# Optimization experiments

Measured on AMD Instinct MI355X. Metric: run time of the kernel, lower is better.

## Reference

```python
import jax, jax.numpy as jnp
import numpy as np

# graph / model dims
N0, N1, N2 = 200000, 50000, 10000   # nodes per sampled layer (src of hop0, src of hop1, targets)
L = 10                               # tokens per node for embedding sum
E0, E1 = 800000, 160000              # edges per hop
V, IN, H, U, LP = 100000, 128, 256, 32, 128  # vocab, in_channels, hidden, unsup_channels, predictor hidden


def _ln(x, g, b, eps=1e-5):
    m = jnp.mean(x, axis=-1, keepdims=True)
    v = jnp.var(x, axis=-1, keepdims=True)
    return (x - m) * jax.lax.rsqrt(v + eps) * g + b


def _lp_edge(e_i, e_j, w1, b1, g, b, w2, b2):
    # LabelPredictor.edge_forward (eval mode: no dropout)
    h = jnp.concatenate([jnp.abs(e_i - e_j), e_i + e_j, e_i * e_j], axis=-1)  # [E, 3U]
    h = jax.nn.relu(_ln(h @ w1.T + b1, g, b))                                  # [E, LP]
    return jax.nn.sigmoid(h @ w2.T + b2)                                       # [E, 1]


def _conv(x_src, x_tgt, src, dst, n_dst, in_c, ll_w, ll_b, lr_w, lp):
    # LAConv.propagate + message, aggr='add', bipartite (x_src, x_tgt)
    xj = x_src[src]                    # gather [E, in_c+U]
    feat_j = xj[:, :in_c]
    un_j = xj[:, in_c:]
    un_i = x_tgt[dst, in_c:]
    A = jax.lax.stop_gradient(_lp_edge(un_i, un_j, *lp))       # [E, 1], frozen predictor
    A_sum = jax.ops.segment_sum(A, dst, num_segments=n_dst)    # softmax-like normalizer
    A = A / A_sum[dst]
    msg = jnp.concatenate([A * feat_j, un_j], axis=-1)         # [E, in_c+U]
    out = jax.ops.segment_sum(msg, dst, num_segments=n_dst)    # scatter-add aggregate
    out_feat = out[:, :in_c] @ ll_w.T + ll_b + x_tgt[:, :in_c] @ lr_w.T
    return jnp.concatenate([out_feat, out[:, in_c:]], axis=-1)


def setup_inputs() -> dict:
    key = jax.random.key(0)
    ks = jax.random.split(key, 24)
    f = lambda k, shape, s=0.02: (jax.random.normal(k, shape, dtype=jnp.float32) * s)
    inp = {
        'x': jax.random.randint(ks[0], (N0, L), 0, V),
        'x_unsup': jax.random.normal(ks[1], (N0, U), dtype=jnp.float32),
        'src0': jax.random.randint(ks[2], (E0,), 0, N0),
        'dst0': jax.random.randint(ks[3], (E0,), 0, N1),
        'src1': jax.random.randint(ks[4], (E1,), 0, N1),
        'dst1': jax.random.randint(ks[5], (E1,), 0, N2),
        'emb_table': f(ks[6], (V, IN), 1.0),
        'ln_g': jnp.ones((IN,), jnp.float32),
        'ln_b': jnp.zeros((IN,), jnp.float32),
        'lp_w1': f(ks[7], (LP, 3 * U), 0.05),
        'lp_b1': jnp.zeros((LP,), jnp.float32),
        'lp_g': jnp.ones((LP,), jnp.float32),
        'lp_bn': jnp.zeros((LP,), jnp.float32),
        'lp_w2': f(ks[8], (1, LP), 0.05),
        'lp_b2': jnp.zeros((1,), jnp.float32),
        'll_w0': f(ks[9], (H, IN)),
        'll_b0': jnp.zeros((H,), jnp.float32),
        'lr_w0': f(ks[10], (H, IN)),
        'll_w1': f(ks[11], (H, H)),
        'll_b1': jnp.zeros((H,), jnp.float32),
        'lr_w1': f(ks[12], (H, H)),
        'out_w': f(ks[13], (1, H)),
        'out_b': jnp.zeros((1,), jnp.float32),
    }
    return inp


def reference(x, x_unsup, src0, dst0, src1, dst1, emb_table, ln_g, ln_b,
              lp_w1, lp_b1, lp_g, lp_bn, lp_w2, lp_b2,
              ll_w0, ll_b0, lr_w0, ll_w1, ll_b1, lr_w1, out_w, out_b):
    lp = (lp_w1, lp_b1, lp_g, lp_bn, lp_w2, lp_b2)
    # embedding with padding_idx=0 (row 0 contributes zero)
    mask = jnp.concatenate([jnp.zeros((1, 1), jnp.float32), jnp.ones((V - 1, 1), jnp.float32)], axis=0)
    table = emb_table * mask
    e = jnp.sum(table[x], axis=1)                 # [N0, IN]
    e = jax.nn.relu(_ln(e, ln_g, ln_b))
    h = jnp.concatenate([e, x_unsup], axis=-1)    # [N0, IN+U]

    # layer 0 (IN -> H)
    h = _conv(h, h[:N1], src0, dst0, N1, IN, ll_w0, ll_b0, lr_w0, lp)
    feat, un = h[:, :H], h[:, H:]
    h = jnp.concatenate([jax.nn.relu(feat), un], axis=-1)  # eval: no dropout

    # layer 1 (H -> H), last layer: no relu
    h = _conv(h, h[:N2], src1, dst1, N2, H, ll_w1, ll_b1, lr_w1, lp)

    return h[:, :H] @ out_w.T + out_b             # [N2, 1]
```

## Files before the change

kernel.cpp:

```cpp
#include <hip/hip_runtime.h>
#include <hip/hip_bf16.h>
#include <math.h>

#define cN0 200000
#define cN1 50000
#define cN2 10000
#define cL  10
#define cE0 800000
#define cE1 160000
#define cV  100000
#define cIN 128
#define cH  256
#define cU  32
#define cLP 128

typedef __attribute__((ext_vector_type(8))) short short8;
typedef __attribute__((ext_vector_type(4))) float floatx4;

__device__ __forceinline__ float wave_sum(float v) {
#pragma unroll
    for (int m = 1; m < 64; m <<= 1) v += __shfl_xor(v, m);
    return v;
}

__device__ __forceinline__ float red16(float v) {
    v += __shfl_xor(v, 1); v += __shfl_xor(v, 2);
    v += __shfl_xor(v, 4); v += __shfl_xor(v, 8);
    return v;
}

__device__ __forceinline__ unsigned short bf16_rne(float f) {
    union { float f; unsigned u; } c; c.f = f;
    unsigned r = (c.u + 0x7FFFu + ((c.u >> 16) & 1u)) >> 16;
    return (unsigned short)r;
}

__device__ __forceinline__ float b2f(unsigned short u) {
    union { unsigned u; float f; } c; c.u = ((unsigned)u) << 16;
    return c.f;
}

__device__ __forceinline__ unsigned pkbf16(float a, float b) {
    union { __hip_bfloat162 h; unsigned u; } c;
    c.h = __float22bfloat162_rn(make_float2(a, b));
    return c.u;
}

__device__ __forceinline__ float2 unpk(unsigned p) {
    union { unsigned u; float f; } lo, hi;
    lo.u = p << 16; hi.u = p & 0xFFFF0000u;
    return make_float2(lo.f, hi.f);
}

__global__ __launch_bounds__(256) void cvt4_kernel(const float* __restrict__ src,
                                                   ushort* __restrict__ dstp)
{
    size_t i = ((size_t)blockIdx.x * 256 + threadIdx.x) * 4;
    float4 v = *(const float4*)&src[i];
    unsigned o0 = pkbf16(v.x, v.y), o1 = pkbf16(v.z, v.w);
    *(uint2*)&dstp[i] = make_uint2(o0, o1);
}

__global__ __launch_bounds__(256) void cvt_w0_kernel(const float* __restrict__ llw0,
                                                     const float* __restrict__ lrw0,
                                                     ushort* __restrict__ Wb)
{
    int idx = blockIdx.x * 256 + threadIdx.x;
    int i = idx * 2;
    int o = i >> 8, k = i & 255;
    float2 v = (k < 128) ? *(const float2*)&llw0[o * 128 + k]
                         : *(const float2*)&lrw0[o * 128 + (k - 128)];
    *(unsigned*)&Wb[i] = pkbf16(v.x, v.y);
}

__global__ __launch_bounds__(256) void embed_kernel(
    const int* __restrict__ x, const ushort* __restrict__ embB,
    const float* __restrict__ g, const float* __restrict__ b,
    ushort* __restrict__ e0)
{
    int wave = threadIdx.x >> 6, lane = threadIdx.x & 63;
    int n = blockIdx.x * 4 + wave;
    const int* xr = x + (size_t)n * cL;
    int toks[cL];
#pragma unroll
    for (int t = 0; t < cL; ++t) toks[t] = xr[t];
    unsigned packed[cL];
#pragma unroll
    for (int t = 0; t < cL; ++t)
        packed[t] = *(const unsigned*)&embB[(size_t)toks[t] * cIN + 2 * lane];
    float ax = 0.f, ay = 0.f;
#pragma unroll
    for (int t = 0; t < cL; ++t) {
        unsigned p = (toks[t] != 0) ? packed[t] : 0u;
        float2 uv = unpk(p);
        ax += uv.x; ay += uv.y;
    }
    float s1 = wave_sum(ax + ay);
    float s2 = wave_sum(ax * ax + ay * ay);
    float mean = s1 * (1.f / cIN);
    float var = s2 * (1.f / cIN) - mean * mean;
    float rstd = rsqrtf(var + 1e-5f);
    float2 gv = *(const float2*)&g[2 * lane];
    float2 bv = *(const float2*)&b[2 * lane];
    float ox = fmaxf((ax - mean) * rstd * gv.x + bv.x, 0.f);
    float oy = fmaxf((ay - mean) * rstd * gv.y + bv.y, 0.f);
    *(unsigned*)&e0[(size_t)n * cIN + 2 * lane] = pkbf16(ox, oy);
}

__global__ void count_kernel(const int* __restrict__ dst, int E, int* __restrict__ cnt)
{
    int e = blockIdx.x * 256 + threadIdx.x;
    if (e < E) atomicAdd(&cnt[dst[e]], 1);
}

__global__ __launch_bounds__(1024) void scan_kernel(const int* __restrict__ cnt,
                                                    int* __restrict__ off, int n)
{
    __shared__ int ps[1024];
    int t = threadIdx.x;
    int chunk = (n + 1023) / 1024;
    int lo = t * chunk;
    int hi = min(lo + chunk, n);
    int s = 0;
    for (int i = lo; i < hi; ++i) s += cnt[i];
    ps[t] = s;
    __syncthreads();
    for (int d = 1; d < 1024; d <<= 1) {
        int v = (t >= d) ? ps[t - d] : 0;
        __syncthreads();
        ps[t] += v;
        __syncthreads();
    }
    int run = ps[t] - s;
    for (int i = lo; i < hi; ++i) { off[i] = run; run += cnt[i]; }
    if (hi == n) off[n] = run;
}

__global__ void scatter_kernel(const int* __restrict__ dst, int E,
                               const int* __restrict__ off, int* __restrict__ pos,
                               int* __restrict__ eid)
{
    int e = blockIdx.x * 256 + threadIdx.x;
    if (e < E) {
        int d = dst[e];
        int p = atomicAdd(&pos[d], 1);
        eid[off[d] + p] = e;
    }
}

__global__ __launch_bounds__(256) void edge_mlp_mfma_kernel(
    const ushort* __restrict__ uni, int stride_i,
    const ushort* __restrict__ unj, int stride_j,
    const int* __restrict__ src, const int* __restrict__ dst, int E,
    const float* __restrict__ w1, const float* __restrict__ b1v,
    const float* __restrict__ gv, const float* __restrict__ bnv,
    const float* __restrict__ w2, const float* __restrict__ b2,
    float* __restrict__ A)
{
    __shared__ float par[cLP * 4];
    int tid = threadIdx.x;
    if (tid < cLP) {
        par[tid * 4 + 0] = b1v[tid];
        par[tid * 4 + 1] = gv[tid];
        par[tid * 4 + 2] = bnv[tid];
        par[tid * 4 + 3] = w2[tid];
    }
    int lane = tid & 63;
    int n = lane & 15, q = lane >> 4;

    union { short8 s; unsigned u[4]; } Bf[8][3];
#pragma unroll
    for (int nt = 0; nt < 8; ++nt) {
#pragma unroll
        for (int c = 0; c < 3; ++c) {
            const float* p = &w1[(size_t)(16 * nt + n) * 96 + 32 * c + 8 * q];
            float4 v0 = *(const float4*)p;
            float4 v1 = *(const float4*)(p + 4);
            Bf[nt][c].u[0] = pkbf16(v0.x, v0.y);
            Bf[nt][c].u[1] = pkbf16(v0.z, v0.w);
            Bf[nt][c].u[2] = pkbf16(v1.x, v1.y);
            Bf[nt][c].u[3] = pkbf16(v1.z, v1.w);
        }
    }
    __syncthreads();
    float b2s = b2[0];

    int wid = blockIdx.x * 4 + (tid >> 6);
    int nw = gridDim.x * 4;
    int ngroups = E >> 4;

    int g = wid;
    int di = 0, si = 0;
    if (g < ngroups) {
        int e = (g << 4) + n;
        di = dst[e]; si = src[e];
    }
    while (g < ngroups) {
        uint4 ivu = *(const uint4*)&uni[(size_t)di * stride_i + 8 * q];
        uint4 jvu = *(const uint4*)&unj[(size_t)si * stride_j + 8 * q];
        int gn = g + nw;
        if (gn < ngroups) {
            int e2 = (gn << 4) + n;
            di = dst[e2]; si = src[e2];
        }
        union { short8 s; unsigned u[4]; } a0, a1, a2;
        {
            unsigned iw[4] = {ivu.x, ivu.y, ivu.z, ivu.w};
            unsigned jw[4] = {jvu.x, jvu.y, jvu.z, jvu.w};
#pragma unroll
            for (int d = 0; d < 4; ++d) {
                float2 u = unpk(iw[d]);
                float2 v = unpk(jw[d]);
                a0.u[d] = pkbf16(fabsf(u.x - v.x), fabsf(u.y - v.y));
                a1.u[d] = pkbf16(u.x + v.x, u.y + v.y);
                a2.u[d] = pkbf16(u.x * v.x, u.y * v.y);
            }
        }
        floatx4 acc[8];
#pragma unroll
        for (int nt = 0; nt < 8; ++nt) acc[nt] = (floatx4){0.f, 0.f, 0.f, 0.f};
#pragma unroll
        for (int nt = 0; nt < 8; ++nt) {
            acc[nt] = __builtin_amdgcn_mfma_f32_16x16x32_bf16(a0.s, Bf[nt][0].s, acc[nt], 0, 0, 0);
            acc[nt] = __builtin_amdgcn_mfma_f32_16x16x32_bf16(a1.s, Bf[nt][1].s, acc[nt], 0, 0, 0);
            acc[nt] = __builtin_amdgcn_mfma_f32_16x16x32_bf16(a2.s, Bf[nt][2].s, acc[nt], 0, 0, 0);
        }
        float s1[4] = {0.f, 0.f, 0.f, 0.f}, s2[4] = {0.f, 0.f, 0.f, 0.f};
#pragma unroll
        for (int nt = 0; nt < 8; ++nt) {
            float4 pp = *(const float4*)&par[(16 * nt + n) * 4];
#pragma unroll
            for (int r = 0; r < 4; ++r) {
                float h = acc[nt][r] + pp.x;
                acc[nt][r] = h;
                s1[r] += h; s2[r] = fmaf(h, h, s2[r]);
            }
        }
        float rstd[4], mrr[4];
#pragma unroll
        for (int r = 0; r < 4; ++r) {
            s1[r] = red16(s1[r]); s2[r] = red16(s2[r]);
            float mean = s1[r] * (1.f / 128.f);
            float var = s2[r] * (1.f / 128.f) - mean * mean;
            rstd[r] = rsqrtf(var + 1e-5f);
            mrr[r] = mean * rstd[r];
        }
        float p[4] = {0.f, 0.f, 0.f, 0.f};
#pragma unroll
        for (int nt = 0; nt < 8; ++nt) {
            float4 pp = *(const float4*)&par[(16 * nt + n) * 4];
#pragma unroll
            for (int r = 0; r < 4; ++r) {
                float z = fmaf(acc[nt][r], rstd[r], -mrr[r]);
                float y = fmaxf(fmaf(z, pp.y, pp.z), 0.f);
                p[r] = fmaf(y, pp.w, p[r]);
            }
        }
#pragma unroll
        for (int r = 0; r < 4; ++r) p[r] = red16(p[r]);
        if (n < 4) {
            float pv = p[n];
            A[(g << 4) + 4 * q + n] = 1.f / (1.f + expf(-(pv + b2s)));
        }
        g = gn;
    }
}

__global__ __launch_bounds__(256) void agg0_kernel(
    const int* __restrict__ off, const int* __restrict__ eid,
    const int* __restrict__ src, const float* __restrict__ A,
    const ushort* __restrict__ e0, const ushort* __restrict__ xub,
    ushort* __restrict__ aggn, ushort* __restrict__ h1b)
{
    int wave = threadIdx.x >> 6, lane = threadIdx.x & 63;
    int i = blockIdx.x * 4 + wave;
    if (i >= cN1) return;
    int s0 = off[i], s1 = off[i + 1];
    bool feat = lane < 32;
    int col = feat ? (4 * lane) : (4 * (lane & 7));
    const ushort* base = feat ? e0 : xub;
    int stride = feat ? cIN : cU;
    float ax = 0.f, ay = 0.f, az = 0.f, aw = 0.f, accA = 0.f;
    int idx = s0;
    for (; idx + 8 <= s1; idx += 8) {
        int ee[8]; float av[8]; int ss[8]; ushort4 vv[8];
#pragma unroll
        for (int t = 0; t < 8; ++t) ee[t] = eid[idx + t];
#pragma unroll
        for (int t = 0; t < 8; ++t) { av[t] = A[ee[t]]; ss[t] = src[ee[t]]; }
#pragma unroll
        for (int t = 0; t < 8; ++t) vv[t] = *(const ushort4*)&base[(size_t)ss[t] * stride + col];
#pragma unroll
        for (int t = 0; t < 8; ++t) {
            float w = feat ? av[t] : 1.f;
            ax = fmaf(w, b2f(vv[t].x), ax); ay = fmaf(w, b2f(vv[t].y), ay);
            az = fmaf(w, b2f(vv[t].z), az); aw = fmaf(w, b2f(vv[t].w), aw);
            accA += av[t];
        }
    }
    for (; idx + 4 <= s1; idx += 4) {
        int ee[4]; float av[4]; int ss[4]; ushort4 vv[4];
#pragma unroll
        for (int t = 0; t < 4; ++t) ee[t] = eid[idx + t];
#pragma unroll
        for (int t = 0; t < 4; ++t) { av[t] = A[ee[t]]; ss[t] = src[ee[t]]; }
#pragma unroll
        for (int t = 0; t < 4; ++t) vv[t] = *(const ushort4*)&base[(size_t)ss[t] * stride + col];
#pragma unroll
        for (int t = 0; t < 4; ++t) {
            float w = feat ? av[t] : 1.f;
            ax = fmaf(w, b2f(vv[t].x), ax); ay = fmaf(w, b2f(vv[t].y), ay);
            az = fmaf(w, b2f(vv[t].z), az); aw = fmaf(w, b2f(vv[t].w), aw);
            accA += av[t];
        }
    }
    for (; idx < s1; ++idx) {
        int e = eid[idx];
        float a = A[e];
        int s = src[e];
        ushort4 v = *(const ushort4*)&base[(size_t)s * stride + col];
        float w = feat ? a : 1.f;
        ax = fmaf(w, b2f(v.x), ax); ay = fmaf(w, b2f(v.y), ay);
        az = fmaf(w, b2f(v.z), az); aw = fmaf(w, b2f(v.w), aw);
        accA += a;
    }
    if (feat) {
        float r = (accA > 0.f) ? (1.f / accA) : 0.f;
        unsigned o0 = pkbf16(ax * r, ay * r), o1 = pkbf16(az * r, aw * r);
        *(uint2*)&aggn[(size_t)i * cIN + col] = make_uint2(o0, o1);
    } else if (lane < 40) {
        unsigned o0 = pkbf16(ax, ay), o1 = pkbf16(az, aw);
        *(uint2*)&h1b[(size_t)i * 288 + 256 + col] = make_uint2(o0, o1);
    }
}

__global__ __launch_bounds__(256) void linear0_mfma_kernel(
    const ushort* __restrict__ aggn, const ushort* __restrict__ e0,
    const ushort* __restrict__ Wb, const float* __restrict__ bias,
    ushort* __restrict__ h1b)
{
    int tid = threadIdx.x;
    int w = tid >> 6, lane = tid & 63;
    int n = lane & 15, q = lane >> 4;
    short8 Bf[4][8];
    float bia[4];
#pragma unroll
    for (int t = 0; t < 4; ++t) {
        int col = 64 * w + 16 * t + n;
        bia[t] = bias[col];
#pragma unroll
        for (int kc = 0; kc < 8; ++kc)
            Bf[t][kc] = *(const short8*)&Wb[(size_t)col * 256 + kc * 32 + 8 * q];
    }
    for (int g = blockIdx.x; g < cN1 / 16; g += gridDim.x) {
        int m0 = g * 16;
        int row = m0 + n;
        short8 Af[8];
#pragma unroll
        for (int kc = 0; kc < 4; ++kc)
            Af[kc] = *(const short8*)&aggn[(size_t)row * cIN + kc * 32 + 8 * q];
#pragma unroll
        for (int kc = 0; kc < 4; ++kc)
            Af[4 + kc] = *(const short8*)&e0[(size_t)row * cIN + kc * 32 + 8 * q];
#pragma unroll
        for (int t = 0; t < 4; ++t) {
            floatx4 acc = {0.f, 0.f, 0.f, 0.f};
#pragma unroll
            for (int kc = 0; kc < 8; ++kc)
                acc = __builtin_amdgcn_mfma_f32_16x16x32_bf16(Af[kc], Bf[t][kc], acc, 0, 0, 0);
            int col = 64 * w + 16 * t + n;
#pragma unroll
            for (int r = 0; r < 4; ++r) {
                int m = m0 + 4 * q + r;
                h1b[(size_t)m * 288 + col] = bf16_rne(fmaxf(acc[r] + bia[t], 0.f));
            }
        }
    }
}

__global__ __launch_bounds__(256) void precompute_kernel(
    const float* __restrict__ ow, const float* __restrict__ llw1,
    const float* __restrict__ lrw1, const float* __restrict__ llb1,
    const float* __restrict__ ob,
    float* __restrict__ v1, float* __restrict__ v2, float* __restrict__ cbuf)
{
    __shared__ float w[256];
    __shared__ float red[256];
    int t = threadIdx.x;
    w[t] = ow[t];
    __syncthreads();
    float s1 = 0.f, s2 = 0.f;
    for (int o = 0; o < 256; ++o) {
        float wo = w[o];
        s1 += wo * llw1[o * 256 + t];
        s2 += wo * lrw1[o * 256 + t];
    }
    v1[t] = s1;
    v2[t] = s2;
    red[t] = w[t] * llb1[t];
    __syncthreads();
    for (int d = 128; d > 0; d >>= 1) {
        if (t < d) red[t] += red[t + d];
        __syncthreads();
    }
    if (t == 0) cbuf[0] = red[0] + ob[0];
}

__global__ __launch_bounds__(256) void agg1_final_kernel(
    const int* __restrict__ off, const int* __restrict__ eid,
    const int* __restrict__ src, const float* __restrict__ A,
    const ushort* __restrict__ h1b, const float* __restrict__ v1,
    const float* __restrict__ v2, const float* __restrict__ cbuf,
    float* __restrict__ out)
{
    int wave = threadIdx.x >> 6, lane = threadIdx.x & 63;
    int n = blockIdx.x * 4 + wave;
    if (n >= cN2) return;
    int s0 = off[n], s1 = off[n + 1];
    float ax = 0.f, ay = 0.f, az = 0.f, aw = 0.f, accA = 0.f;
    int idx = s0;
    for (; idx + 8 <= s1; idx += 8) {
        int ee[8]; float av[8]; int ss[8]; ushort4 vv[8];
#pragma unroll
        for (int t = 0; t < 8; ++t) ee[t] = eid[idx + t];
#pragma unroll
        for (int t = 0; t < 8; ++t) { av[t] = A[ee[t]]; ss[t] = src[ee[t]]; }
#pragma unroll
        for (int t = 0; t < 8; ++t) vv[t] = *(const ushort4*)&h1b[(size_t)ss[t] * 288 + 4 * lane];
#pragma unroll
        for (int t = 0; t < 8; ++t) {
            ax = fmaf(av[t], b2f(vv[t].x), ax); ay = fmaf(av[t], b2f(vv[t].y), ay);
            az = fmaf(av[t], b2f(vv[t].z), az); aw = fmaf(av[t], b2f(vv[t].w), aw);
            accA += av[t];
        }
    }
    for (; idx + 4 <= s1; idx += 4) {
        int ee[4]; float av[4]; int ss[4]; ushort4 vv[4];
#pragma unroll
        for (int t = 0; t < 4; ++t) ee[t] = eid[idx + t];
#pragma unroll
        for (int t = 0; t < 4; ++t) { av[t] = A[ee[t]]; ss[t] = src[ee[t]]; }
#pragma unroll
        for (int t = 0; t < 4; ++t) vv[t] = *(const ushort4*)&h1b[(size_t)ss[t] * 288 + 4 * lane];
#pragma unroll
        for (int t = 0; t < 4; ++t) {
            ax = fmaf(av[t], b2f(vv[t].x), ax); ay = fmaf(av[t], b2f(vv[t].y), ay);
            az = fmaf(av[t], b2f(vv[t].z), az); aw = fmaf(av[t], b2f(vv[t].w), aw);
            accA += av[t];
        }
    }
    for (; idx < s1; ++idx) {
        int e = eid[idx];
        float a = A[e];
        int s = src[e];
        ushort4 v = *(const ushort4*)&h1b[(size_t)s * 288 + 4 * lane];
        ax = fmaf(a, b2f(v.x), ax); ay = fmaf(a, b2f(v.y), ay);
        az = fmaf(a, b2f(v.z), az); aw = fmaf(a, b2f(v.w), aw);
        accA += a;
    }
    float r = (accA > 0.f) ? (1.f / accA) : 0.f;
    ushort4 t4 = *(const ushort4*)&h1b[(size_t)n * 288 + 4 * lane];
    float4 w1v = *(const float4*)&v1[4 * lane];
    float4 w2v = *(const float4*)&v2[4 * lane];
    float p = r * (ax * w1v.x + ay * w1v.y + az * w1v.z + aw * w1v.w)
            + b2f(t4.x) * w2v.x + b2f(t4.y) * w2v.y
            + b2f(t4.z) * w2v.z + b2f(t4.w) * w2v.w;
    p = wave_sum(p);
    if (lane == 0) out[n] = p + cbuf[0];
}

extern "C" void kernel_launch(void* const* d_in, const int* in_sizes, int n_in,
                              void* d_out, int out_size, void* d_ws, size_t ws_size,
                              hipStream_t stream)
{
    const int*   x     = (const int*)d_in[0];
    const float* xu    = (const float*)d_in[1];
    const int*   src0  = (const int*)d_in[2];
    const int*   dst0  = (const int*)d_in[3];
    const int*   src1  = (const int*)d_in[4];
    const int*   dst1  = (const int*)d_in[5];
    const float* emb   = (const float*)d_in[6];
    const float* ln_g  = (const float*)d_in[7];
    const float* ln_b  = (const float*)d_in[8];
    const float* lp_w1 = (const float*)d_in[9];
    const float* lp_b1 = (const float*)d_in[10];
    const float* lp_g  = (const float*)d_in[11];
    const float* lp_bn = (const float*)d_in[12];
    const float* lp_w2 = (const float*)d_in[13];
    const float* lp_b2 = (const float*)d_in[14];
    const float* ll_w0 = (const float*)d_in[15];
    const float* ll_b0 = (const float*)d_in[16];
    const float* lr_w0 = (const float*)d_in[17];
    const float* ll_w1 = (const float*)d_in[18];
    const float* ll_b1 = (const float*)d_in[19];
    const float* lr_w1 = (const float*)d_in[20];
    const float* out_w = (const float*)d_in[21];
    const float* out_b = (const float*)d_in[22];
    float* out = (float*)d_out;

    char* ws = (char*)d_ws;
    size_t off = 0;
    auto alloc = [&](size_t bytes) -> void* {
        void* p = ws + off;
        off = (off + bytes + 255) & ~(size_t)255;
        return p;
    };
    ushort* embB = (ushort*)alloc((size_t)cV * cIN * 2);
    ushort* xub  = (ushort*)alloc((size_t)cN0 * cU * 2);
    ushort* e0   = (ushort*)alloc((size_t)cN0 * cIN * 2);
    ushort* aggn = (ushort*)alloc((size_t)cN1 * cIN * 2);
    ushort* h1b  = (ushort*)alloc((size_t)cN1 * 288 * 2);
    float* A0    = (float*)alloc((size_t)cE0 * 4);
    float* A1    = (float*)alloc((size_t)cE1 * 4);
    ushort* Wb   = (ushort*)alloc((size_t)256 * 256 * 2);
    float* v1    = (float*)alloc(256 * 4);
    float* v2    = (float*)alloc(256 * 4);
    float* cbuf  = (float*)alloc(64);
    int* cnt0    = (int*)alloc((size_t)cN1 * 4);
    int* off0    = (int*)alloc((size_t)(cN1 + 1) * 4);
    int* pos0    = (int*)alloc((size_t)cN1 * 4);
    int* eid0    = (int*)alloc((size_t)cE0 * 4);
    int* cnt1    = (int*)alloc((size_t)cN2 * 4);
    int* off1    = (int*)alloc((size_t)(cN2 + 1) * 4);
    int* pos1    = (int*)alloc((size_t)cN2 * 4);
    int* eid1    = (int*)alloc((size_t)cE1 * 4);

    hipMemsetAsync(cnt0, 0, (size_t)cN1 * 4, stream);
    hipMemsetAsync(pos0, 0, (size_t)cN1 * 4, stream);
    hipMemsetAsync(cnt1, 0, (size_t)cN2 * 4, stream);
    hipMemsetAsync(pos1, 0, (size_t)cN2 * 4, stream);

    cvt4_kernel<<<(cV * cIN) / 1024, 256, 0, stream>>>(emb, embB);
    cvt4_kernel<<<(cN0 * cU) / 1024, 256, 0, stream>>>(xu, xub);
    cvt_w0_kernel<<<128, 256, 0, stream>>>(ll_w0, lr_w0, Wb);

    embed_kernel<<<cN0 / 4, 256, 0, stream>>>(x, embB, ln_g, ln_b, e0);

    count_kernel<<<(cE0 + 255) / 256, 256, 0, stream>>>(dst0, cE0, cnt0);
    scan_kernel<<<1, 1024, 0, stream>>>(cnt0, off0, cN1);
    scatter_kernel<<<(cE0 + 255) / 256, 256, 0, stream>>>(dst0, cE0, off0, pos0, eid0);

    edge_mlp_mfma_kernel<<<1024, 256, 0, stream>>>(xub, cU, xub, cU, src0, dst0, cE0,
                                                   lp_w1, lp_b1, lp_g, lp_bn, lp_w2, lp_b2, A0);

    agg0_kernel<<<(cN1 + 3) / 4, 256, 0, stream>>>(off0, eid0, src0, A0, e0, xub, aggn, h1b);

    linear0_mfma_kernel<<<784, 256, 0, stream>>>(aggn, e0, Wb, ll_b0, h1b);

    count_kernel<<<(cE1 + 255) / 256, 256, 0, stream>>>(dst1, cE1, cnt1);
    scan_kernel<<<1, 1024, 0, stream>>>(cnt1, off1, cN2);
    scatter_kernel<<<(cE1 + 255) / 256, 256, 0, stream>>>(dst1, cE1, off1, pos1, eid1);

    edge_mlp_mfma_kernel<<<512, 256, 0, stream>>>(h1b + 256, 288, h1b + 256, 288, src1, dst1, cE1,
                                                  lp_w1, lp_b1, lp_g, lp_bn, lp_w2, lp_b2, A1);

    precompute_kernel<<<1, 256, 0, stream>>>(out_w, ll_w1, lr_w1, ll_b1, out_b, v1, v2, cbuf);

    agg1_final_kernel<<<(cN2 + 3) / 4, 256, 0, stream>>>(off1, eid1, src1, A1, h1b, v1, v2, cbuf, out);
}
```

Baseline: 677.8 us.

## Batch CSR build for both hops, merge conversions, parallelize precompute and scan

Merges the two bf16 conversion launches into one kernel and the four memsets into one contiguous memset. Builds the CSR (count, scan, scatter) for both hops in single launches, with the scan using two blocks and vectorized tiled loads instead of a serial per-thread chunk loop. Spreads the weight-folding precompute across 65 blocks using wave reductions instead of one serial block. The aim is fewer launches and less serial latency, at the cost of more branching inside the fused kernels.

```diff
diff --git a/kernel.cpp b/kernel.cpp
--- a/kernel.cpp
+++ b/kernel.cpp
@@ -52,13 +52,21 @@
     return make_float2(lo.f, hi.f);
 }
 
-__global__ __launch_bounds__(256) void cvt4_kernel(const float* __restrict__ src,
-                                                   ushort* __restrict__ dstp)
+__global__ __launch_bounds__(256) void cvt_all_kernel(const float* __restrict__ emb,
+                                                      const float* __restrict__ xu,
+                                                      ushort* __restrict__ embB,
+                                                      ushort* __restrict__ xub)
 {
     size_t i = ((size_t)blockIdx.x * 256 + threadIdx.x) * 4;
-    float4 v = *(const float4*)&src[i];
+    const size_t nEmb = (size_t)cV * cIN;
+    const float* s;
+    ushort* d;
+    size_t j;
+    if (i < nEmb) { s = emb; d = embB; j = i; }
+    else { s = xu; d = xub; j = i - nEmb; if (j >= (size_t)cN0 * cU) return; }
+    float4 v = *(const float4*)&s[j];
     unsigned o0 = pkbf16(v.x, v.y), o1 = pkbf16(v.z, v.w);
-    *(uint2*)&dstp[i] = make_uint2(o0, o1);
+    *(uint2*)&d[j] = make_uint2(o0, o1);
 }
 
 __global__ __launch_bounds__(256) void cvt_w0_kernel(const float* __restrict__ llw0,
@@ -107,44 +115,97 @@
     *(unsigned*)&e0[(size_t)n * cIN + 2 * lane] = pkbf16(ox, oy);
 }
 
-__global__ void count_kernel(const int* __restrict__ dst, int E, int* __restrict__ cnt)
+__global__ void count_kernel(const int* __restrict__ dst0, const int* __restrict__ dst1,
+                             int* __restrict__ cnt0, int* __restrict__ cnt1)
 {
     int e = blockIdx.x * 256 + threadIdx.x;
-    if (e < E) atomicAdd(&cnt[dst[e]], 1);
-}
-
-__global__ __launch_bounds__(1024) void scan_kernel(const int* __restrict__ cnt,
-                                                    int* __restrict__ off, int n)
-{
+    if (e < cE0) {
+        atomicAdd(&cnt0[dst0[e]], 1);
+    } else {
+        int e1 = e - cE0;
+        if (e1 < cE1) atomicAdd(&cnt1[dst1[e1]], 1);
+    }
+}
+
+__global__ __launch_bounds__(1024) void scan_kernel(const int* __restrict__ cnt0,
+                                                    int* __restrict__ off0,
+                                                    const int* __restrict__ cnt1,
+                                                    int* __restrict__ off1)
+{
+    const int* cnt = blockIdx.x ? cnt1 : cnt0;
+    int* off = blockIdx.x ? off1 : off0;
+    int n = blockIdx.x ? cN2 : cN1;
     __shared__ int ps[1024];
+    __shared__ int carrySh;
     int t = threadIdx.x;
-    int chunk = (n + 1023) / 1024;
-    int lo = t * chunk;
-    int hi = min(lo + chunk, n);
-    int s = 0;
-    for (int i = lo; i < hi; ++i) s += cnt[i];
-    ps[t] = s;
+    if (t == 0) carrySh = 0;
     __syncthreads();
-    for (int d = 1; d < 1024; d <<= 1) {
-        int v = (t >= d) ? ps[t - d] : 0;
+    int ntile = (n + 16383) >> 14;
+    for (int tl = 0; tl < ntile; ++tl) {
+        int i0 = (tl << 14) + t * 16;
+        int v[16];
+        if (i0 + 16 <= n) {
+            int4 a = *(const int4*)&cnt[i0];
+            int4 bq = *(const int4*)&cnt[i0 + 4];
+            int4 c = *(const int4*)&cnt[i0 + 8];
+            int4 d = *(const int4*)&cnt[i0 + 12];
+            v[0] = a.x; v[1] = a.y; v[2] = a.z; v[3] = a.w;
+            v[4] = bq.x; v[5] = bq.y; v[6] = bq.z; v[7] = bq.w;
+            v[8] = c.x; v[9] = c.y; v[10] = c.z; v[11] = c.w;
+            v[12] = d.x; v[13] = d.y; v[14] = d.z; v[15] = d.w;
+        } else {
+#pragma unroll
+            for (int k = 0; k < 16; ++k) v[k] = (i0 + k < n) ? cnt[i0 + k] : 0;
+        }
+        int s = 0;
+#pragma unroll
+        for (int k = 0; k < 16; ++k) s += v[k];
+        ps[t] = s;
         __syncthreads();
-        ps[t] += v;
+        for (int d = 1; d < 1024; d <<= 1) {
+            int x = (t >= d) ? ps[t - d] : 0;
+            __syncthreads();
+            ps[t] += x;
+            __syncthreads();
+        }
+        int run = ps[t] - s + carrySh;
+        if (i0 + 16 <= n) {
+            int w[16];
+#pragma unroll
+            for (int k = 0; k < 16; ++k) { w[k] = run; run += v[k]; }
+            *(int4*)&off[i0]      = make_int4(w[0], w[1], w[2], w[3]);
+            *(int4*)&off[i0 + 4]  = make_int4(w[4], w[5], w[6], w[7]);
+            *(int4*)&off[i0 + 8]  = make_int4(w[8], w[9], w[10], w[11]);
+            *(int4*)&off[i0 + 12] = make_int4(w[12], w[13], w[14], w[15]);
+        } else {
+#pragma unroll
+            for (int k = 0; k < 16; ++k)
+                if (i0 + k < n) { off[i0 + k] = run; run += v[k]; }
+        }
         __syncthreads();
-    }
-    int run = ps[t] - s;
-    for (int i = lo; i < hi; ++i) { off[i] = run; run += cnt[i]; }
-    if (hi == n) off[n] = run;
-}
-
-__global__ void scatter_kernel(const int* __restrict__ dst, int E,
-                               const int* __restrict__ off, int* __restrict__ pos,
-                               int* __restrict__ eid)
+        if (t == 1023) carrySh += ps[1023];
+        __syncthreads();
+    }
+    if (t == 0) off[n] = carrySh;
+}
+
+__global__ void scatter_kernel(const int* __restrict__ dst0, const int* __restrict__ dst1,
+                               const int* __restrict__ off0, const int* __restrict__ off1,
+                               int* __restrict__ pos0, int* __restrict__ pos1,
+                               int* __restrict__ eid0, int* __restrict__ eid1)
 {
     int e = blockIdx.x * 256 + threadIdx.x;
-    if (e < E) {
-        int d = dst[e];
-        int p = atomicAdd(&pos[d], 1);
-        eid[off[d] + p] = e;
+    if (e < cE0) {
+        int d = dst0[e];
+        int p = atomicAdd(&pos0[d], 1);
+        eid0[off0[d] + p] = e;
+    } else {
+        int e1 = e - cE0;
+        if (e1 < cE1) {
+            int d = dst1[e1];
+            int p = atomicAdd(&pos1[d], 1);
+            eid1[off1[d] + p] = e1;
+        }
     }
 }
 
@@ -384,26 +445,30 @@
     const float* __restrict__ ob,
     float* __restrict__ v1, float* __restrict__ v2, float* __restrict__ cbuf)
 {
-    __shared__ float w[256];
-    __shared__ float red[256];
-    int t = threadIdx.x;
-    w[t] = ow[t];
-    __syncthreads();
-    float s1 = 0.f, s2 = 0.f;
-    for (int o = 0; o < 256; ++o) {
-        float wo = w[o];
-        s1 += wo * llw1[o * 256 + t];
-        s2 += wo * lrw1[o * 256 + t];
-    }
-    v1[t] = s1;
-    v2[t] = s2;
-    red[t] = w[t] * llb1[t];
-    __syncthreads();
-    for (int d = 128; d > 0; d >>= 1) {
-        if (t < d) red[t] += red[t + d];
-        __syncthreads();
-    }
-    if (t == 0) cbuf[0] = red[0] + ob[0];
+    int b = blockIdx.x;
+    int wave = threadIdx.x >> 6, lane = threadIdx.x & 63;
+    if (b < 64) {
+        int t = b * 4 + wave;
+        float s1 = 0.f, s2 = 0.f;
+#pragma unroll
+        for (int k = 0; k < 4; ++k) {
+            int o = lane + 64 * k;
+            float wo = ow[o];
+            s1 = fmaf(wo, llw1[o * 256 + t], s1);
+            s2 = fmaf(wo, lrw1[o * 256 + t], s2);
+        }
+        s1 = wave_sum(s1); s2 = wave_sum(s2);
+        if (lane == 0) { v1[t] = s1; v2[t] = s2; }
+    } else if (wave == 0) {
+        float s = 0.f;
+#pragma unroll
+        for (int k = 0; k < 4; ++k) {
+            int t = lane + 64 * k;
+            s = fmaf(ow[t], llb1[t], s);
+        }
+        s = wave_sum(s);
+        if (lane == 0) cbuf[0] = s + ob[0];
+    }
 }
 
 __global__ __launch_bounds__(256) void agg1_final_kernel(
@@ -516,29 +581,29 @@
     float* v1    = (float*)alloc(256 * 4);
     float* v2    = (float*)alloc(256 * 4);
     float* cbuf  = (float*)alloc(64);
+    char* zbase  = ws + off;
     int* cnt0    = (int*)alloc((size_t)cN1 * 4);
+    int* pos0    = (int*)alloc((size_t)cN1 * 4);
+    int* cnt1    = (int*)alloc((size_t)cN2 * 4);
+    int* pos1    = (int*)alloc((size_t)cN2 * 4);
+    size_t zlen  = (size_t)((ws + off) - zbase);
     int* off0    = (int*)alloc((size_t)(cN1 + 1) * 4);
-    int* pos0    = (int*)alloc((size_t)cN1 * 4);
+    int* off1    = (int*)alloc((size_t)(cN2 + 1) * 4);
     int* eid0    = (int*)alloc((size_t)cE0 * 4);
-    int* cnt1    = (int*)alloc((size_t)cN2 * 4);
-    int* off1    = (int*)alloc((size_t)(cN2 + 1) * 4);
-    int* pos1    = (int*)alloc((size_t)cN2 * 4);
     int* eid1    = (int*)alloc((size_t)cE1 * 4);
 
-    hipMemsetAsync(cnt0, 0, (size_t)cN1 * 4, stream);
-    hipMemsetAsync(pos0, 0, (size_t)cN1 * 4, stream);
-    hipMemsetAsync(cnt1, 0, (size_t)cN2 * 4, stream);
-    hipMemsetAsync(pos1, 0, (size_t)cN2 * 4, stream);
-
-    cvt4_kernel<<<(cV * cIN) / 1024, 256, 0, stream>>>(emb, embB);
-    cvt4_kernel<<<(cN0 * cU) / 1024, 256, 0, stream>>>(xu, xub);
+    hipMemsetAsync(zbase, 0, zlen, stream);
+
+    cvt_all_kernel<<<(cV * cIN + cN0 * cU) / 1024, 256, 0, stream>>>(emb, xu, embB, xub);
     cvt_w0_kernel<<<128, 256, 0, stream>>>(ll_w0, lr_w0, Wb);
+    precompute_kernel<<<65, 256, 0, stream>>>(out_w, ll_w1, lr_w1, ll_b1, out_b, v1, v2, cbuf);
 
     embed_kernel<<<cN0 / 4, 256, 0, stream>>>(x, embB, ln_g, ln_b, e0);
 
-    count_kernel<<<(cE0 + 255) / 256, 256, 0, stream>>>(dst0, cE0, cnt0);
-    scan_kernel<<<1, 1024, 0, stream>>>(cnt0, off0, cN1);
-    scatter_kernel<<<(cE0 + 255) / 256, 256, 0, stream>>>(dst0, cE0, off0, pos0, eid0);
+    count_kernel<<<(cE0 + cE1 + 255) / 256, 256, 0, stream>>>(dst0, dst1, cnt0, cnt1);
+    scan_kernel<<<2, 1024, 0, stream>>>(cnt0, off0, cnt1, off1);
+    scatter_kernel<<<(cE0 + cE1 + 255) / 256, 256, 0, stream>>>(dst0, dst1, off0, off1,
+                                                                pos0, pos1, eid0, eid1);
 
     edge_mlp_mfma_kernel<<<1024, 256, 0, stream>>>(xub, cU, xub, cU, src0, dst0, cE0,
                                                    lp_w1, lp_b1, lp_g, lp_bn, lp_w2, lp_b2, A0);
@@ -547,14 +612,8 @@
 
     linear0_mfma_kernel<<<784, 256, 0, stream>>>(aggn, e0, Wb, ll_b0, h1b);
 
-    count_kernel<<<(cE1 + 255) / 256, 256, 0, stream>>>(dst1, cE1, cnt1);
-    scan_kernel<<<1, 1024, 0, stream>>>(cnt1, off1, cN2);
-    scatter_kernel<<<(cE1 + 255) / 256, 256, 0, stream>>>(dst1, cE1, off1, pos1, eid1);
-
     edge_mlp_mfma_kernel<<<512, 256, 0, stream>>>(h1b + 256, 288, h1b + 256, 288, src1, dst1, cE1,
                                                   lp_w1, lp_b1, lp_g, lp_bn, lp_w2, lp_b2, A1);
 
-    precompute_kernel<<<1, 256, 0, stream>>>(out_w, ll_w1, lr_w1, ll_b1, out_b, v1, v2, cbuf);
-
     agg1_final_kernel<<<(cN2 + 3) / 4, 256, 0, stream>>>(off1, eid1, src1, A1, h1b, v1, v2, cbuf, out);
 }
```

Measured after the change: 581.2 us. 14.3% less time.
